# Performance work log

Hardware: AMD Instinct MI355X
Metric: run time of the kernel (lower is better)

The kernel has to match this reference:

```python
import jax, jax.numpy as jnp
import numpy as np

N_NODES = 50000
N_EDGES = 800000
D = 128


def setup_inputs() -> dict:
    key = jax.random.key(0)
    k1, k2, k3, k4, k5 = jax.random.split(key, 5)
    graph_embedding = jax.random.normal(k1, (N_NODES, D), dtype=jnp.float32)
    weight = jax.random.normal(k2, (1, D), dtype=jnp.float32)
    src = jax.random.randint(k3, (N_EDGES,), 0, N_NODES, dtype=jnp.int32)
    dst = jax.random.randint(k4, (N_EDGES,), 0, N_NODES, dtype=jnp.int32)
    e_feat = jax.random.randint(k5, (N_EDGES,), 0, 8, dtype=jnp.int32)
    return {"graph_embedding": graph_embedding, "weight": weight,
            "src": src, "dst": dst, "e_feat": e_feat}


def reference(graph_embedding, weight, src, dst, e_feat):
    n = graph_embedding.shape[0]
    # emb, emb0, emb2, emb4, emb6 are all graph_embedding * self.weight in the original.
    emb = graph_embedding * weight                      # [N, D]
    msg = emb[src]                                      # [E, D] gathered source features
    # update_all(message_func, sum): plain scatter-sum of src features to dst.
    res = jax.ops.segment_sum(msg, dst, num_segments=n)  # [N, D]
    # Original calls message_func0 (mask e==0) for ft0, ft2, ft4 AND ft6.
    e = e_feat.reshape(-1, 1).astype(jnp.float32)       # [E, 1]
    msg0 = jnp.where(e == 0.0, msg, jnp.zeros_like(msg))
    res0 = jax.ops.segment_sum(msg0, dst, num_segments=n)
    return (res, res0, res0, res0, res0)
```

## Files before the change

### kernel.cpp

```cpp
#include <hip/hip_runtime.h>

constexpr int N_NODES = 50000;
constexpr int N_EDGES = 800000;
constexpr int D = 128;
constexpr int CAP = 64;

__global__ void fill_kernel(const int* __restrict__ src,
                            const int* __restrict__ dst,
                            const int* __restrict__ ef,
                            int* __restrict__ counts,
                            int* __restrict__ slots) {
    int e = blockIdx.x * blockDim.x + threadIdx.x;
    if (e < N_EDGES) {
        int t = dst[e];
        int pos = atomicAdd(&counts[t], 1);
        if (pos < CAP)
            slots[(size_t)t * CAP + pos] = src[e] | ((ef[e] == 0) ? 0x80000000 : 0);
    }
}

__global__ void accumulate_slots_kernel(const float* __restrict__ emb,
                                        const float* __restrict__ w,
                                        const int* __restrict__ counts,
                                        const int* __restrict__ slots,
                                        float* __restrict__ out) {
    int lane = threadIdx.x & 63;
    int wave = (blockIdx.x * blockDim.x + threadIdx.x) >> 6;
    int n_waves = (gridDim.x * blockDim.x) >> 6;
    const size_t ND = (size_t)N_NODES * D;
    float2 wv = ((const float2*)w)[lane];

    for (int n = wave; n < N_NODES; n += n_waves) {
        int cnt = __builtin_nontemporal_load(counts + n);
        if (cnt > CAP) cnt = CAP;
        int pk_lane = __builtin_nontemporal_load(slots + (size_t)n * CAP + lane);
        float2 acc  = make_float2(0.f, 0.f);
        float2 acc0 = make_float2(0.f, 0.f);
        for (int j = 0; j < cnt; ++j) {
            int pk = __shfl(pk_lane, j, 64);
            int s  = pk & 0x7fffffff;
            float2 v = ((const float2*)(emb + (size_t)s * D))[lane];
            acc.x += v.x;  acc.y += v.y;
            if (pk < 0) { acc0.x += v.x; acc0.y += v.y; }
        }
        acc.x  *= wv.x; acc.y  *= wv.y;
        acc0.x *= wv.x; acc0.y *= wv.y;
        float* o = out + (size_t)n * D + lane * 2;
        __builtin_nontemporal_store(acc.x,  o);
        __builtin_nontemporal_store(acc.y,  o + 1);
        __builtin_nontemporal_store(acc0.x, o + ND);
        __builtin_nontemporal_store(acc0.y, o + ND + 1);
        __builtin_nontemporal_store(acc0.x, o + 2 * ND);
        __builtin_nontemporal_store(acc0.y, o + 2 * ND + 1);
        __builtin_nontemporal_store(acc0.x, o + 3 * ND);
        __builtin_nontemporal_store(acc0.y, o + 3 * ND + 1);
        __builtin_nontemporal_store(acc0.x, o + 4 * ND);
        __builtin_nontemporal_store(acc0.y, o + 4 * ND + 1);
    }
}

extern "C" void kernel_launch(void* const* d_in, const int* in_sizes, int n_in,
                              void* d_out, int out_size, void* d_ws, size_t ws_size,
                              hipStream_t stream) {
    const float* emb = (const float*)d_in[0];
    const float* w   = (const float*)d_in[1];
    const int*   src = (const int*)d_in[2];
    const int*   dst = (const int*)d_in[3];
    const int*   ef  = (const int*)d_in[4];
    float* out = (float*)d_out;

    int* counts = (int*)d_ws;
    int* slots  = counts + 50048;

    hipMemsetAsync(counts, 0, N_NODES * sizeof(int), stream);

    fill_kernel<<<(N_EDGES + 255) / 256, 256, 0, stream>>>(src, dst, ef, counts, slots);

    accumulate_slots_kernel<<<2048, 256, 0, stream>>>(emb, w, counts, slots, out);
}
```

Measured before the change: 266.0 us.

## Slice-transpose embedding, pack slots to 16-bit with flag bitmasks, gather per slice

Transposes the embedding into 8 column slices of 16 floats, so each slice table is small and contiguous and gathers within a slice stay cache-local. Each wave now handles 8 nodes at once, with 8 lanes per node and one slice per block. This gives more independent loads in flight than one node per wave. Source indices are packed to 16 bits and the e==0 mask moves to a per-node bitmask set with atomicOr, which shrinks slot traffic. The cost is an extra transpose pass over the whole embedding, which runs only if the workspace is large enough, plus extra atomics in the fill kernel.

```diff
diff --git a/kernel.cpp b/kernel.cpp
--- a/kernel.cpp
+++ b/kernel.cpp
@@ -5,58 +5,93 @@
 constexpr int D = 128;
 constexpr int CAP = 64;
 
+typedef float v2f __attribute__((ext_vector_type(2)));
+
+__global__ void transpose_kernel(const float* __restrict__ emb,
+                                 float* __restrict__ embT) {
+    int tid = blockIdx.x * blockDim.x + threadIdx.x;
+    if (tid >= N_NODES * 32) return;
+    int n  = tid >> 5;
+    int r  = tid & 31;
+    int s  = r >> 2;
+    int kq = r & 3;
+    float4 v = *(const float4*)(emb + (size_t)n * D + s * 16 + kq * 4);
+    *(float4*)(embT + ((size_t)s * N_NODES + n) * 16 + kq * 4) = v;
+}
+
 __global__ void fill_kernel(const int* __restrict__ src,
                             const int* __restrict__ dst,
                             const int* __restrict__ ef,
                             int* __restrict__ counts,
-                            int* __restrict__ slots) {
+                            unsigned short* __restrict__ slots,
+                            unsigned int* __restrict__ flags) {
     int e = blockIdx.x * blockDim.x + threadIdx.x;
     if (e < N_EDGES) {
         int t = dst[e];
         int pos = atomicAdd(&counts[t], 1);
-        if (pos < CAP)
-            slots[(size_t)t * CAP + pos] = src[e] | ((ef[e] == 0) ? 0x80000000 : 0);
+        if (pos < CAP) {
+            slots[(size_t)t * CAP + pos] = (unsigned short)src[e];
+            if (ef[e] == 0)
+                atomicOr(&flags[t * 2 + (pos >> 5)], 1u << (pos & 31));
+        }
     }
 }
 
-__global__ void accumulate_slots_kernel(const float* __restrict__ emb,
-                                        const float* __restrict__ w,
-                                        const int* __restrict__ counts,
-                                        const int* __restrict__ slots,
-                                        float* __restrict__ out) {
-    int lane = threadIdx.x & 63;
-    int wave = (blockIdx.x * blockDim.x + threadIdx.x) >> 6;
-    int n_waves = (gridDim.x * blockDim.x) >> 6;
+template<bool TRANS>
+__global__ void accumulate_kernel(const float* __restrict__ tab,
+                                  const float* __restrict__ w,
+                                  const int* __restrict__ counts,
+                                  const unsigned int* __restrict__ slots2,
+                                  const uint2* __restrict__ flags,
+                                  float* __restrict__ out) {
+    int slice = blockIdx.x & 7;
+    int og    = blockIdx.x >> 3;
+    int wid   = threadIdx.x >> 6;
+    int lane  = threadIdx.x & 63;
+    int g     = lane >> 3;
+    int l8    = lane & 7;
+    int octet = og * 4 + wid;
+    if (octet >= N_NODES / 8) return;
+    int n = octet * 8 + g;
+
+    int c = counts[n]; if (c > CAP) c = CAP;
+    uint2 fl = flags[n];
+    const unsigned* sp = slots2 + (size_t)n * 32;
+    unsigned p0 = sp[l8], p1 = sp[l8 + 8], p2 = sp[l8 + 16], p3 = sp[l8 + 24];
+
+    const float* base = TRANS ? tab + (size_t)slice * N_NODES * 16
+                              : tab + slice * 16;
+    float accx = 0.f, accy = 0.f, acc0x = 0.f, acc0y = 0.f;
+    int gl = g << 3;
+
+    auto chunk = [&](unsigned preg, int jbase, unsigned flw) {
+        int je = c - jbase; if (je > 16) je = 16;
+        for (int jj = 0; jj < je; ++jj) {
+            unsigned pr = (unsigned)__shfl((int)preg, gl + (jj >> 1), 64);
+            int s = (jj & 1) ? (int)(pr >> 16) : (int)(pr & 0xffffu);
+            const float* ap = TRANS ? base + (size_t)s * 16 + (l8 << 1)
+                                    : base + (size_t)s * D + (l8 << 1);
+            v2f v = *(const v2f*)ap;
+            accx += v.x; accy += v.y;
+            if ((flw >> jj) & 1) { acc0x += v.x; acc0y += v.y; }
+        }
+    };
+    chunk(p0,  0, fl.x);
+    chunk(p1, 16, fl.x >> 16);
+    chunk(p2, 32, fl.y);
+    chunk(p3, 48, fl.y >> 16);
+
+    v2f wv = *(const v2f*)(w + slice * 16 + (l8 << 1));
+    v2f a, a0;
+    a.x  = accx  * wv.x;  a.y  = accy  * wv.y;
+    a0.x = acc0x * wv.x;  a0.y = acc0y * wv.y;
     const size_t ND = (size_t)N_NODES * D;
-    float2 wv = ((const float2*)w)[lane];
-
-    for (int n = wave; n < N_NODES; n += n_waves) {
-        int cnt = __builtin_nontemporal_load(counts + n);
-        if (cnt > CAP) cnt = CAP;
-        int pk_lane = __builtin_nontemporal_load(slots + (size_t)n * CAP + lane);
-        float2 acc  = make_float2(0.f, 0.f);
-        float2 acc0 = make_float2(0.f, 0.f);
-        for (int j = 0; j < cnt; ++j) {
-            int pk = __shfl(pk_lane, j, 64);
-            int s  = pk & 0x7fffffff;
-            float2 v = ((const float2*)(emb + (size_t)s * D))[lane];
-            acc.x += v.x;  acc.y += v.y;
-            if (pk < 0) { acc0.x += v.x; acc0.y += v.y; }
-        }
-        acc.x  *= wv.x; acc.y  *= wv.y;
-        acc0.x *= wv.x; acc0.y *= wv.y;
-        float* o = out + (size_t)n * D + lane * 2;
-        __builtin_nontemporal_store(acc.x,  o);
-        __builtin_nontemporal_store(acc.y,  o + 1);
-        __builtin_nontemporal_store(acc0.x, o + ND);
-        __builtin_nontemporal_store(acc0.y, o + ND + 1);
-        __builtin_nontemporal_store(acc0.x, o + 2 * ND);
-        __builtin_nontemporal_store(acc0.y, o + 2 * ND + 1);
-        __builtin_nontemporal_store(acc0.x, o + 3 * ND);
-        __builtin_nontemporal_store(acc0.y, o + 3 * ND + 1);
-        __builtin_nontemporal_store(acc0.x, o + 4 * ND);
-        __builtin_nontemporal_store(acc0.y, o + 4 * ND + 1);
-    }
+    float* o = out + (size_t)n * D + slice * 16 + (l8 << 1);
+    __builtin_nontemporal_store(a,  (v2f*)o);
+    __builtin_nontemporal_store(a0, (v2f*)(o + ND));
+    __builtin_nontemporal_store(a0, (v2f*)(o + 2 * ND));
+    __builtin_nontemporal_store(a0, (v2f*)(o + 3 * ND));
+    __builtin_nontemporal_store(a0, (v2f*)(o + 4 * ND));
 }
 
 extern "C" void kernel_launch(void* const* d_in, const int* in_sizes, int n_in,
@@ -69,12 +104,24 @@
     const int*   ef  = (const int*)d_in[4];
     float* out = (float*)d_out;
 
-    int* counts = (int*)d_ws;
-    int* slots  = counts + 50048;
+    char* wsb = (char*)d_ws;
+    int*            counts = (int*)wsb;
+    unsigned int*   flags  = (unsigned int*)(wsb + 200192);
+    unsigned short* slots  = (unsigned short*)(wsb + 600576);
+    float*          embT   = (float*)(wsb + 7000832);
+    const bool trans = (ws_size >= 32600832);
 
-    hipMemsetAsync(counts, 0, N_NODES * sizeof(int), stream);
+    hipMemsetAsync(counts, 0, 600576, stream);
 
-    fill_kernel<<<(N_EDGES + 255) / 256, 256, 0, stream>>>(src, dst, ef, counts, slots);
+    if (trans)
+        transpose_kernel<<<6250, 256, 0, stream>>>(emb, embT);
 
-    accumulate_slots_kernel<<<2048, 256, 0, stream>>>(emb, w, counts, slots, out);
+    fill_kernel<<<3125, 256, 0, stream>>>(src, dst, ef, counts, slots, flags);
+
+    if (trans)
+        accumulate_kernel<true><<<12504, 256, 0, stream>>>(embT, w, counts,
+            (const unsigned int*)slots, (const uint2*)flags, out);
+    else
+        accumulate_kernel<false><<<12504, 256, 0, stream>>>(emb, w, counts,
+            (const unsigned int*)slots, (const uint2*)flags, out);
 }
```

After: 283.4 us. +6.6%, slower.
